# Performance work log

Measured on AMD Instinct MI355X. Metric: run time of the kernel, lower is better.

Reference implementation:

```python
import jax, jax.numpy as jnp
import numpy as np

D_IN = 512
HLS = [1024, 1024, 512]
N_Q = 4096
N_K = 16384
N_CLASSES = 100
BN_EPS = 1e-5


def _bn(x, gamma, beta):
    # BatchNorm1d in training mode: per-batch mean/biased-var normalization
    m = jnp.mean(x, axis=0)
    v = jnp.var(x, axis=0)
    return gamma * (x - m) * jax.lax.rsqrt(v + BN_EPS) + beta


def _neg_cdist(a, b):
    # -||a_i - b_j||_2 via expanded form (GEMM-dominated)
    a2 = jnp.sum(a * a, axis=1, keepdims=True)          # [N,1]
    b2 = jnp.sum(b * b, axis=1, keepdims=True).T        # [1,M]
    d2 = a2 + b2 - 2.0 * (a @ b.T)                      # [N,M]
    return -jnp.sqrt(jnp.maximum(d2, 0.0))


def setup_inputs() -> dict:
    key = jax.random.key(0)
    ks = jax.random.split(key, 32)
    inp = {
        "x": jax.random.normal(ks[0], (N_Q, D_IN), jnp.float32),
        "x_n": jax.random.normal(ks[1], (N_K, D_IN), jnp.float32),
        "y_n": jax.random.randint(ks[2], (N_K,), 0, N_CLASSES, jnp.int32),
        "in_gamma": jnp.ones((D_IN,), jnp.float32),
        "in_beta": jnp.zeros((D_IN,), jnp.float32),
    }
    dims = [D_IN] + HLS
    ki = 3
    for i in range(len(HLS)):
        fan_in = dims[i]
        bound = 1.0 / np.sqrt(fan_in)
        inp[f"W{i}"] = jax.random.uniform(ks[ki], (dims[i + 1], dims[i]), jnp.float32, -bound, bound); ki += 1
        inp[f"b{i}"] = jax.random.uniform(ks[ki], (dims[i + 1],), jnp.float32, -bound, bound); ki += 1
        inp[f"g{i}"] = jnp.ones((dims[i + 1],), jnp.float32)
        inp[f"bt{i}"] = jnp.zeros((dims[i + 1],), jnp.float32)
    return inp


def reference(x, x_n, y_n, in_gamma, in_beta,
              W0, b0, g0, bt0, W1, b1, g1, bt1, W2, b2, g2, bt2):
    x = _bn(x, in_gamma, in_beta)
    x_n = _bn(x_n, in_gamma, in_beta)
    layers = [(W0, b0, g0, bt0), (W1, b1, g1, bt1), (W2, b2, g2, bt2)]
    for W, b, g, bt in layers:
        x = _bn(jnp.tanh(x @ W.T + b), g, bt)
        x_n = _bn(jnp.tanh(x_n @ W.T + b), g, bt)
    sim = _neg_cdist(x, x_n)                       # [N_Q, N_K]
    scores = jax.nn.softmax(sim, axis=1)
    y_ohe = jax.nn.one_hot(y_n, N_CLASSES, dtype=x.dtype)  # [N_K, C]
    return jnp.clip(scores @ y_ohe, 0.0, 1.0)
```

## Files before the change

kernel.cpp:

```cpp
#include <hip/hip_runtime.h>
#include <math.h>

#define NQ 4096
#define NK 16384
#define NROWS 20480
#define NCLS 100
#define PCLS 112
#define DCH 16

typedef __attribute__((ext_vector_type(8))) short bf16x8;
typedef __attribute__((ext_vector_type(4))) float f32x4;

__device__ inline unsigned short f2bf(float f) {
  unsigned u = __float_as_uint(f);
  u += 0x7fff + ((u >> 16) & 1);
  return (unsigned short)(u >> 16);
}
__device__ inline void upk(unsigned u, float& a, float& b) {
  a = __uint_as_float(u << 16);
  b = __uint_as_float(u & 0xffff0000u);
}
__device__ inline float fast_tanh(float x) {
  float e = __expf(2.f * x);
  return 1.f - 2.f / (e + 1.f);
}
__device__ inline void gload_lds16(const unsigned short* g, unsigned short* l) {
  __builtin_amdgcn_global_load_lds(
      (const __attribute__((address_space(1))) unsigned int*)g,
      (__attribute__((address_space(3))) unsigned int*)l, 16, 0, 0);
}

__global__ __launch_bounds__(256) void conv_bf16(
    const float* __restrict__ in, unsigned short* __restrict__ outp, size_t n4) {
  size_t i = (size_t)blockIdx.x * 256 + threadIdx.x;
  size_t stride = (size_t)gridDim.x * 256;
  for (; i < n4; i += stride) {
    float4 v = ((const float4*)in)[i];
    unsigned lo = (unsigned)f2bf(v.x) | ((unsigned)f2bf(v.y) << 16);
    unsigned hi = (unsigned)f2bf(v.z) | ((unsigned)f2bf(v.w) << 16);
    ((uint2*)outp)[i] = make_uint2(lo, hi);
  }
}

__global__ __launch_bounds__(256) void colstats_part_f(
    const float* __restrict__ A, int D, int rpc, float* __restrict__ part) {
  int j = blockIdx.x * 256 + threadIdx.x;
  int c = blockIdx.y;
  const float* p = A + (size_t)c * rpc * D + j;
  float s = 0.f, s2 = 0.f;
#pragma unroll 4
  for (int r = 0; r < rpc; ++r) {
    float v = p[(size_t)r * D];
    s += v; s2 += v * v;
  }
  part[(size_t)c * 2 * D + j] = s;
  part[(size_t)c * 2 * D + D + j] = s2;
}

__global__ __launch_bounds__(256) void finish_ab(
    const float* __restrict__ part, int D, float invN,
    const float* __restrict__ g, const float* __restrict__ bt,
    float* __restrict__ ab) {
  int j = blockIdx.x * 256 + threadIdx.x;
  if (j >= D) return;
  float s = 0.f, s2 = 0.f;
  for (int c = 0; c < 64; ++c) {
    s += part[(size_t)c * 2 * D + j];
    s2 += part[(size_t)c * 2 * D + D + j];
  }
  float m = s * invN;
  float v = fmaxf(s2 * invN - m * m, 0.f);
  float a = g[j] * rsqrtf(v + 1e-5f);
  ab[2 * j] = a;
  ab[2 * j + 1] = bt[j] - a * m;
}

__global__ __launch_bounds__(256) void ab_from_stats(
    const float* __restrict__ st, const float* __restrict__ g,
    const float* __restrict__ bt, float invN, float* __restrict__ ab, int M) {
  int j = blockIdx.x * 256 + threadIdx.x;
  if (j >= M) return;
  float s = st[2 * j], s2 = st[2 * j + 1];
  float m = s * invN;
  float v = fmaxf(s2 * invN - m * m, 0.f);
  float a = g[j] * rsqrtf(v + 1e-5f);
  ab[2 * j] = a;
  ab[2 * j + 1] = bt[j] - a * m;
}

__global__ __launch_bounds__(256) void fold_w(
    const float* __restrict__ W, const float* __restrict__ b,
    const float* __restrict__ ab, int K,
    unsigned short* __restrict__ Wo, float* __restrict__ bo) {
  int j = blockIdx.x;
  int t = threadIdx.x;
  const float* Wr = W + (size_t)j * K;
  unsigned short* Wor = Wo + (size_t)j * K;
  float s = 0.f;
  for (int k = t; k < K; k += 256) {
    float w = Wr[k];
    Wor[k] = f2bf(ab[2 * k] * w);
    s += ab[2 * k + 1] * w;
  }
  __shared__ float red[4];
#pragma unroll
  for (int off = 32; off; off >>= 1) s += __shfl_down(s, off, 64);
  if ((t & 63) == 0) red[t >> 6] = s;
  __syncthreads();
  if (t == 0) bo[j] = b[j] + red[0] + red[1] + red[2] + red[3];
}

__global__ __launch_bounds__(256) void gemm_v6(
    const unsigned short* __restrict__ A, const unsigned short* __restrict__ W,
    const float* __restrict__ bias, unsigned short* __restrict__ C,
    float* __restrict__ st, int M, int K) {
  __shared__ unsigned short As[4][128 * 32];
  __shared__ unsigned short Ws[4][128 * 32];
  int tid = threadIdx.x;
  int l = tid & 63, w = tid >> 6;
  int rowBase = blockIdx.y * 128, colBase = blockIdx.x * 128;
  int rowOff = (w >> 1) * 64, colOff = (w & 1) * 64;
  int fr = l & 15, fc = l >> 4;

  const unsigned short* Ag[2];
  const unsigned short* Wg[2];
  int slot[2];
#pragma unroll
  for (int j = 0; j < 2; ++j) {
    int i = tid + j * 256;
    int r = i >> 2, c = (i & 3) ^ (r & 3);
    slot[j] = i * 8;
    Ag[j] = A + (size_t)(rowBase + r) * K + c * 8;
    Wg[j] = W + (size_t)(colBase + r) * K + c * 8;
  }
  auto stage = [&](int s, int bb) {
    int ko = s * 32;
#pragma unroll
    for (int j = 0; j < 2; ++j) {
      gload_lds16(Ag[j] + ko, &As[bb][0] + slot[j]);
      gload_lds16(Wg[j] + ko, &Ws[bb][0] + slot[j]);
    }
  };

  f32x4 acc[4][4];
#pragma unroll
  for (int m = 0; m < 4; ++m)
#pragma unroll
    for (int n = 0; n < 4; ++n) acc[m][n] = (f32x4){0.f, 0.f, 0.f, 0.f};

  int NS = K >> 5;
  stage(0, 0);
  stage(1, 1);
  stage(2, 2);
  for (int s = 0; s < NS; ++s) {
    if (s + 2 < NS) {
      asm volatile("s_waitcnt vmcnt(8)" ::: "memory");
    } else if (s + 1 < NS) {
      asm volatile("s_waitcnt vmcnt(4)" ::: "memory");
    } else {
      asm volatile("s_waitcnt vmcnt(0)" ::: "memory");
    }
    __builtin_amdgcn_s_barrier();
    __builtin_amdgcn_sched_barrier(0);
    int b = s & 3;
    bf16x8 av[4], bv[4];
#pragma unroll
    for (int m = 0; m < 4; ++m) {
      int row = rowOff + m * 16 + fr;
      int p = fc ^ (row & 3);
      av[m] = *(const bf16x8*)((const char*)&As[b][0] + row * 64 + p * 16);
    }
#pragma unroll
    for (int n = 0; n < 4; ++n) {
      int row = colOff + n * 16 + fr;
      int p = fc ^ (row & 3);
      bv[n] = *(const bf16x8*)((const char*)&Ws[b][0] + row * 64 + p * 16);
    }
    if (s + 3 < NS) stage(s + 3, (s + 3) & 3);
#pragma unroll
    for (int m = 0; m < 4; ++m)
#pragma unroll
      for (int n = 0; n < 4; ++n)
        acc[m][n] = __builtin_amdgcn_mfma_f32_16x16x32_bf16(av[m], bv[n], acc[m][n], 0, 0, 0);
  }

  float ts1[4] = {0.f, 0.f, 0.f, 0.f};
  float ts2[4] = {0.f, 0.f, 0.f, 0.f};
#pragma unroll
  for (int m = 0; m < 4; ++m) {
#pragma unroll
    for (int r = 0; r < 4; ++r) {
      size_t row = rowBase + rowOff + m * 16 + fc * 4 + r;
      unsigned short* Crow = C + row * M;
#pragma unroll
      for (int n = 0; n < 4; ++n) {
        int col = colBase + colOff + n * 16 + fr;
        float val = fast_tanh(acc[m][n][r] + bias[col]);
        Crow[col] = f2bf(val);
        ts1[n] += val;
        ts2[n] += val * val;
      }
    }
  }
#pragma unroll
  for (int n = 0; n < 4; ++n) {
    float s1 = ts1[n], s2 = ts2[n];
    s1 += __shfl_xor(s1, 16, 64); s1 += __shfl_xor(s1, 32, 64);
    s2 += __shfl_xor(s2, 16, 64); s2 += __shfl_xor(s2, 32, 64);
    if (fc == 0) {
      int col = colBase + colOff + n * 16 + fr;
      atomicAdd(&st[2 * col], s1);
      atomicAdd(&st[2 * col + 1], s2);
    }
  }
}

__global__ __launch_bounds__(256) void bn_final(
    unsigned short* __restrict__ F, const float* __restrict__ ab,
    float* __restrict__ norms) {
  int w = threadIdx.x >> 6, l = threadIdx.x & 63;
  int row = blockIdx.x * 4 + w;
  unsigned short* p = F + (size_t)row * 512 + l * 8;
  uint4 v = *(const uint4*)p;
  int j0 = l * 8;
  float f[8];
  upk(v.x, f[0], f[1]); upk(v.y, f[2], f[3]);
  upk(v.z, f[4], f[5]); upk(v.w, f[6], f[7]);
  float s = 0.f;
  unsigned pk[4];
#pragma unroll
  for (int e = 0; e < 8; e += 2) {
    float a0 = ab[2 * (j0 + e)] * f[e] + ab[2 * (j0 + e) + 1];
    float a1 = ab[2 * (j0 + e + 1)] * f[e + 1] + ab[2 * (j0 + e + 1) + 1];
    s += a0 * a0 + a1 * a1;
    pk[e >> 1] = (unsigned)f2bf(a0) | ((unsigned)f2bf(a1) << 16);
  }
  *(uint4*)p = make_uint4(pk[0], pk[1], pk[2], pk[3]);
#pragma unroll
  for (int off = 32; off; off >>= 1) s += __shfl_down(s, off, 64);
  if (l == 0) norms[row] = s;
}

__global__ __launch_bounds__(256) void scatter_ohe(
    const int* __restrict__ yn, unsigned short* __restrict__ oheT) {
  int k = blockIdx.x * 256 + threadIdx.x;
  if (k < NK) oheT[(size_t)yn[k] * NK + k] = 0x3F80;
}

__global__ __launch_bounds__(512, 2) void dist_v5(
    const unsigned short* __restrict__ F,
    const float* __restrict__ norms,
    const unsigned short* __restrict__ oheT,
    float* __restrict__ part) {
  __shared__ unsigned short kbuf[3][128 * 64];
  __shared__ unsigned short Qs[8 * 64 * 64];
  __shared__ unsigned short Ps[64][136];
  __shared__ float k2s[1024];
  int tid = threadIdx.x;
  int l = tid & 63, w = tid >> 6;
  int qBase = blockIdx.x * 64;
  int kBase0 = blockIdx.y * 1024;
  int mg = w & 1, ng = w >> 1;
  int qtw = w & 3, cth = w >> 2;
  int fr = l & 15, fc = l >> 4;

  for (int i = tid; i < 1024; i += 512) k2s[i] = norms[NQ + kBase0 + i];
  float q2r0 = norms[qBase + mg * 32 + fr];
  float q2r1 = norms[qBase + mg * 32 + 16 + fr];
  __builtin_amdgcn_sched_barrier(0);

#pragma unroll
  for (int j = 0; j < 8; ++j) {
    int i = tid + j * 512;
    int ss = i >> 9;
    int row = (i >> 3) & 63;
    int c = (i & 7) ^ (row & 7);
    gload_lds16(F + (size_t)(qBase + row) * 512 + ss * 64 + c * 8, Qs + i * 8);
  }

  int i0 = tid, i1 = tid + 512;
  int r0 = i0 >> 3, c0 = (i0 & 7) ^ (r0 & 7);
  int r1 = i1 >> 3, c1 = (i1 & 7) ^ (r1 & 7);
  auto stage = [&](int slice, int bb) {
    int kRow = kBase0 + (slice >> 3) * 128;
    int ko = (slice & 7) * 64;
    gload_lds16(F + (size_t)(NQ + kRow + r0) * 512 + ko + c0 * 8,
                &kbuf[bb][0] + i0 * 8);
    gload_lds16(F + (size_t)(NQ + kRow + r1) * 512 + ko + c1 * 8,
                &kbuf[bb][0] + i1 * 8);
  };

  f32x4 accC[4];
#pragma unroll
  for (int c = 0; c < 4; ++c) accC[c] = (f32x4){0.f, 0.f, 0.f, 0.f};

  stage(0, 0);
  stage(1, 1);
  asm volatile("s_waitcnt lgkmcnt(0)" ::: "memory");

  for (int kt = 0; kt < 8; ++kt) {
    f32x4 acc[2][2];
#pragma unroll
    for (int t2 = 0; t2 < 2; ++t2)
#pragma unroll
      for (int qt = 0; qt < 2; ++qt) acc[t2][qt] = (f32x4){0.f, 0.f, 0.f, 0.f};
    bf16x8 ob[4][4];
#pragma unroll
    for (int kc = 0; kc < 4; ++kc)
#pragma unroll
      for (int c = 0; c < 4; ++c) ob[kc][c] = (bf16x8){0, 0, 0, 0, 0, 0, 0, 0};
#pragma unroll
    for (int s = 0; s < 8; ++s) {
      int slice = kt * 8 + s;
      if (slice == 63) {
        asm volatile("s_waitcnt vmcnt(0)" ::: "memory");
      } else if (s == 1 || s == 2) {
        asm volatile("s_waitcnt vmcnt(18)" ::: "memory");
      } else {
        asm volatile("s_waitcnt vmcnt(2)" ::: "memory");
      }
      __builtin_amdgcn_s_barrier();
      __builtin_amdgcn_sched_barrier(0);
      int b = slice % 3;
      bf16x8 kv[2][2];
#pragma unroll
      for (int kc = 0; kc < 2; ++kc)
#pragma unroll
        for (int t2 = 0; t2 < 2; ++t2) {
          int row = ng * 32 + t2 * 16 + fr;
          int sl = (kc * 4 + fc) ^ (row & 7);
          kv[kc][t2] = *(const bf16x8*)((const char*)&kbuf[b][0] + row * 128 + sl * 16);
        }
      bf16x8 avx[2][2];
#pragma unroll
      for (int kc = 0; kc < 2; ++kc)
#pragma unroll
        for (int qt = 0; qt < 2; ++qt) {
          int row = mg * 32 + qt * 16 + fr;
          int sl = (kc * 4 + fc) ^ (fr & 7);
          avx[kc][qt] = *(const bf16x8*)((const char*)Qs + s * 8192 + row * 128 + sl * 16);
        }
      if (slice + 2 < 64) stage(slice + 2, (slice + 2) % 3);
      if (s == 0) {
        __builtin_amdgcn_sched_barrier(0);
#pragma unroll
        for (int kc = 0; kc < 4; ++kc)
#pragma unroll
          for (int c = 0; c < 4; ++c) {
            int ctg = cth * 4 + c;
            if (ctg < 7)
              ob[kc][c] = *(const bf16x8*)(
                  oheT + (size_t)(ctg * 16 + fr) * NK + kBase0 + kt * 128 + kc * 32 + fc * 8);
          }
        __builtin_amdgcn_sched_barrier(0);
      }
#pragma unroll
      for (int kc = 0; kc < 2; ++kc)
#pragma unroll
        for (int t2 = 0; t2 < 2; ++t2)
#pragma unroll
          for (int qt = 0; qt < 2; ++qt)
            acc[t2][qt] = __builtin_amdgcn_mfma_f32_16x16x32_bf16(
                kv[kc][t2], avx[kc][qt], acc[t2][qt], 0, 0, 0);
    }
#pragma unroll
    for (int t2 = 0; t2 < 2; ++t2) {
      float k2v[4];
#pragma unroll
      for (int r = 0; r < 4; ++r)
        k2v[r] = k2s[kt * 128 + ng * 32 + t2 * 16 + fc * 4 + r];
#pragma unroll
      for (int qt = 0; qt < 2; ++qt) {
        int q = mg * 32 + qt * 16 + fr;
        float q2 = qt ? q2r1 : q2r0;
        float pv[4];
#pragma unroll
        for (int r = 0; r < 4; ++r) {
          float d2 = q2 + k2v[r] - 2.f * acc[t2][qt][r];
          pv[r] = __expf(-sqrtf(fmaxf(d2, 0.f)));
        }
        unsigned lo = (unsigned)f2bf(pv[0]) | ((unsigned)f2bf(pv[1]) << 16);
        unsigned hi = (unsigned)f2bf(pv[2]) | ((unsigned)f2bf(pv[3]) << 16);
        *(uint2*)(&Ps[q][ng * 32 + t2 * 16 + fc * 4]) = make_uint2(lo, hi);
      }
    }
    asm volatile("s_waitcnt lgkmcnt(0)" ::: "memory");
    __builtin_amdgcn_s_barrier();
    __builtin_amdgcn_sched_barrier(0);
#pragma unroll
    for (int kc = 0; kc < 4; ++kc) {
      bf16x8 pa = *(const bf16x8*)(&Ps[qtw * 16 + fr][kc * 32 + fc * 8]);
#pragma unroll
      for (int c = 0; c < 4; ++c) {
        int ctg = cth * 4 + c;
        if (ctg < 7)
          accC[c] = __builtin_amdgcn_mfma_f32_16x16x32_bf16(pa, ob[kc][c], accC[c], 0, 0, 0);
      }
    }
  }
#pragma unroll
  for (int c = 0; c < 4; ++c) {
    int ctg = cth * 4 + c;
    if (ctg < 7) {
#pragma unroll
      for (int r = 0; r < 4; ++r) {
        int q = qBase + qtw * 16 + fc * 4 + r;
        part[((size_t)q * DCH + blockIdx.y) * PCLS + ctg * 16 + fr] = accC[c][r];
      }
    }
  }
}

__global__ __launch_bounds__(128) void combine_out(
    const float* __restrict__ part, float* __restrict__ outp) {
  int q = blockIdx.x;
  int t = threadIdx.x;
  float num = 0.f;
  if (t < NCLS) {
#pragma unroll
    for (int ch = 0; ch < DCH; ++ch)
      num += part[((size_t)q * DCH + ch) * PCLS + t];
  }
  __shared__ float sn[128];
  sn[t] = (t < NCLS) ? num : 0.f;
  __syncthreads();
#pragma unroll
  for (int off = 64; off; off >>= 1) {
    if (t < off) sn[t] += sn[t + off];
    __syncthreads();
  }
  float L = sn[0];
  if (t < NCLS) outp[(size_t)q * NCLS + t] = fminf(fmaxf(num / L, 0.f), 1.f);
}

extern "C" void kernel_launch(void* const* d_in, const int* in_sizes, int n_in,
                              void* d_out, int out_size, void* d_ws, size_t ws_size,
                              hipStream_t stream) {
  (void)in_sizes; (void)n_in; (void)out_size; (void)ws_size;
  const float* x   = (const float*)d_in[0];
  const float* xn  = (const float*)d_in[1];
  const int*   yn  = (const int*)d_in[2];
  const float* ing = (const float*)d_in[3];
  const float* inb = (const float*)d_in[4];
  const float* Wl[3]  = {(const float*)d_in[5], (const float*)d_in[9],  (const float*)d_in[13]};
  const float* bl[3]  = {(const float*)d_in[6], (const float*)d_in[10], (const float*)d_in[14]};
  const float* gl[3]  = {(const float*)d_in[7], (const float*)d_in[11], (const float*)d_in[15]};
  const float* btl[3] = {(const float*)d_in[8], (const float*)d_in[12], (const float*)d_in[16]};
  float* outp = (float*)d_out;

  unsigned short* featA = (unsigned short*)d_ws;
  unsigned short* featB = featA + (size_t)NROWS * 1024;
  unsigned short* wq  = featB + (size_t)NROWS * 1024;
  unsigned short* wk  = wq + (size_t)1024 * 1024;
  unsigned short* ohe = wk + (size_t)1024 * 1024;
  float* spart = (float*)(ohe + (size_t)PCLS * NK);
  float* abq   = spart + 64 * 2 * 512;
  float* abk   = abq + 2048;
  float* statq = abk + 2048;
  float* statk = statq + 2048;
  float* bpq   = statk + 2048;
  float* bpk   = bpq + 1024;
  float* norms = bpk + 1024;
  float* part  = norms + NROWS;

  colstats_part_f<<<dim3(2, 64), 256, 0, stream>>>(x, 512, NQ / 64, spart);
  finish_ab<<<2, 256, 0, stream>>>(spart, 512, 1.0f / NQ, ing, inb, abq);
  colstats_part_f<<<dim3(2, 64), 256, 0, stream>>>(xn, 512, NK / 64, spart);
  finish_ab<<<2, 256, 0, stream>>>(spart, 512, 1.0f / NK, ing, inb, abk);

  conv_bf16<<<1024, 256, 0, stream>>>(x, featA, (size_t)NQ * 512 / 4);
  conv_bf16<<<2048, 256, 0, stream>>>(xn, featA + (size_t)NQ * 512, (size_t)NK * 512 / 4);

  hipMemsetAsync(ohe, 0, (size_t)PCLS * NK * sizeof(unsigned short), stream);
  scatter_ohe<<<NK / 256, 256, 0, stream>>>(yn, ohe);

  int dims[4] = {512, 1024, 1024, 512};
  unsigned short *src = featA, *dst = featB;
  for (int lyr = 0; lyr < 3; ++lyr) {
    int K = dims[lyr], M = dims[lyr + 1];
    fold_w<<<M, 256, 0, stream>>>(Wl[lyr], bl[lyr], abq, K, wq, bpq);
    fold_w<<<M, 256, 0, stream>>>(Wl[lyr], bl[lyr], abk, K, wk, bpk);
    hipMemsetAsync(statq, 0, (size_t)M * 2 * sizeof(float), stream);
    hipMemsetAsync(statk, 0, (size_t)M * 2 * sizeof(float), stream);
    gemm_v6<<<dim3(M / 128, NQ / 128), 256, 0, stream>>>(src, wq, bpq, dst, statq, M, K);
    gemm_v6<<<dim3(M / 128, NK / 128), 256, 0, stream>>>(
        src + (size_t)NQ * K, wk, bpk, dst + (size_t)NQ * M, statk, M, K);
    ab_from_stats<<<M / 256, 256, 0, stream>>>(statq, gl[lyr], btl[lyr], 1.0f / NQ, abq, M);
    ab_from_stats<<<M / 256, 256, 0, stream>>>(statk, gl[lyr], btl[lyr], 1.0f / NK, abk, M);
    unsigned short* t = src; src = dst; dst = t;
  }
  bn_final<<<NQ / 4, 256, 0, stream>>>(src, abq, norms);
  bn_final<<<NK / 4, 256, 0, stream>>>(src + (size_t)NQ * 512, abk, norms + NQ);

  dist_v5<<<dim3(NQ / 64, DCH), 512, 0, stream>>>(src, norms, ohe, part);
  combine_out<<<NQ, 128, 0, stream>>>(part, outp);
}
```

Baseline: 566.2 us.

## Restructure GEMM and distance main loops to process two K-slices per barrier

Both the MLP GEMM and the distance kernel now wait for all outstanding loads and synchronise once per pair of K-slices instead of once per slice. Each pair issues the next two slice prefetches right after the barrier, then runs a larger MFMA burst under raised wave priority (s_setprio). The distance kernel grows its K buffer from three to four stages and replaces the predicated one-hot loads with clamped unconditional loads. The GEMM also gains a launch bound of two blocks per SM. The aim is fewer barriers and longer uninterrupted MFMA runs, at the cost of a shallower effective prefetch lead (vmcnt(0) every pair), more registers and more LDS.

```diff
diff --git a/kernel.cpp b/kernel.cpp
--- a/kernel.cpp
+++ b/kernel.cpp
@@ -110,7 +110,7 @@
   if (t == 0) bo[j] = b[j] + red[0] + red[1] + red[2] + red[3];
 }
 
-__global__ __launch_bounds__(256) void gemm_v6(
+__global__ __launch_bounds__(256, 2) void gemm_v6(
     const unsigned short* __restrict__ A, const unsigned short* __restrict__ W,
     const float* __restrict__ bias, unsigned short* __restrict__ C,
     float* __restrict__ st, int M, int K) {
@@ -148,40 +148,45 @@
 #pragma unroll
     for (int n = 0; n < 4; ++n) acc[m][n] = (f32x4){0.f, 0.f, 0.f, 0.f};
 
-  int NS = K >> 5;
+  int NP = K >> 6;
   stage(0, 0);
   stage(1, 1);
-  stage(2, 2);
-  for (int s = 0; s < NS; ++s) {
-    if (s + 2 < NS) {
-      asm volatile("s_waitcnt vmcnt(8)" ::: "memory");
-    } else if (s + 1 < NS) {
-      asm volatile("s_waitcnt vmcnt(4)" ::: "memory");
-    } else {
-      asm volatile("s_waitcnt vmcnt(0)" ::: "memory");
-    }
+  for (int P = 0; P < NP; ++P) {
+    asm volatile("s_waitcnt vmcnt(0)" ::: "memory");
     __builtin_amdgcn_s_barrier();
     __builtin_amdgcn_sched_barrier(0);
-    int b = s & 3;
-    bf16x8 av[4], bv[4];
-#pragma unroll
-    for (int m = 0; m < 4; ++m) {
-      int row = rowOff + m * 16 + fr;
-      int p = fc ^ (row & 3);
-      av[m] = *(const bf16x8*)((const char*)&As[b][0] + row * 64 + p * 16);
-    }
-#pragma unroll
-    for (int n = 0; n < 4; ++n) {
-      int row = colOff + n * 16 + fr;
-      int p = fc ^ (row & 3);
-      bv[n] = *(const bf16x8*)((const char*)&Ws[b][0] + row * 64 + p * 16);
-    }
-    if (s + 3 < NS) stage(s + 3, (s + 3) & 3);
-#pragma unroll
-    for (int m = 0; m < 4; ++m)
-#pragma unroll
-      for (int n = 0; n < 4; ++n)
-        acc[m][n] = __builtin_amdgcn_mfma_f32_16x16x32_bf16(av[m], bv[n], acc[m][n], 0, 0, 0);
+    if (P + 1 < NP) {
+      stage(2 * P + 2, (2 * P + 2) & 3);
+      stage(2 * P + 3, (2 * P + 3) & 3);
+    }
+    __builtin_amdgcn_sched_barrier(0);
+    bf16x8 av[2][4], bv[2][4];
+#pragma unroll
+    for (int sl2 = 0; sl2 < 2; ++sl2) {
+      int b = (2 * P + sl2) & 3;
+#pragma unroll
+      for (int m = 0; m < 4; ++m) {
+        int row = rowOff + m * 16 + fr;
+        int p = fc ^ (row & 3);
+        av[sl2][m] = *(const bf16x8*)((const char*)&As[b][0] + row * 64 + p * 16);
+      }
+#pragma unroll
+      for (int n = 0; n < 4; ++n) {
+        int row = colOff + n * 16 + fr;
+        int p = fc ^ (row & 3);
+        bv[sl2][n] = *(const bf16x8*)((const char*)&Ws[b][0] + row * 64 + p * 16);
+      }
+    }
+    __builtin_amdgcn_s_setprio(1);
+#pragma unroll
+    for (int sl2 = 0; sl2 < 2; ++sl2)
+#pragma unroll
+      for (int m = 0; m < 4; ++m)
+#pragma unroll
+        for (int n = 0; n < 4; ++n)
+          acc[m][n] = __builtin_amdgcn_mfma_f32_16x16x32_bf16(
+              av[sl2][m], bv[sl2][n], acc[m][n], 0, 0, 0);
+    __builtin_amdgcn_s_setprio(0);
   }
 
   float ts1[4] = {0.f, 0.f, 0.f, 0.f};
@@ -252,7 +257,7 @@
     const float* __restrict__ norms,
     const unsigned short* __restrict__ oheT,
     float* __restrict__ part) {
-  __shared__ unsigned short kbuf[3][128 * 64];
+  __shared__ unsigned short kbuf[4][128 * 64];
   __shared__ unsigned short Qs[8 * 64 * 64];
   __shared__ unsigned short Ps[64][136];
   __shared__ float k2s[1024];
@@ -306,62 +311,60 @@
       for (int qt = 0; qt < 2; ++qt) acc[t2][qt] = (f32x4){0.f, 0.f, 0.f, 0.f};
     bf16x8 ob[4][4];
 #pragma unroll
-    for (int kc = 0; kc < 4; ++kc)
-#pragma unroll
-      for (int c = 0; c < 4; ++c) ob[kc][c] = (bf16x8){0, 0, 0, 0, 0, 0, 0, 0};
-#pragma unroll
-    for (int s = 0; s < 8; ++s) {
-      int slice = kt * 8 + s;
-      if (slice == 63) {
-        asm volatile("s_waitcnt vmcnt(0)" ::: "memory");
-      } else if (s == 1 || s == 2) {
-        asm volatile("s_waitcnt vmcnt(18)" ::: "memory");
-      } else {
-        asm volatile("s_waitcnt vmcnt(2)" ::: "memory");
-      }
+    for (int P = 0; P < 4; ++P) {
+      int gp = kt * 4 + P;
+      asm volatile("s_waitcnt vmcnt(0)" ::: "memory");
       __builtin_amdgcn_s_barrier();
       __builtin_amdgcn_sched_barrier(0);
-      int b = slice % 3;
-      bf16x8 kv[2][2];
-#pragma unroll
-      for (int kc = 0; kc < 2; ++kc)
-#pragma unroll
-        for (int t2 = 0; t2 < 2; ++t2) {
-          int row = ng * 32 + t2 * 16 + fr;
-          int sl = (kc * 4 + fc) ^ (row & 7);
-          kv[kc][t2] = *(const bf16x8*)((const char*)&kbuf[b][0] + row * 128 + sl * 16);
-        }
-      bf16x8 avx[2][2];
-#pragma unroll
-      for (int kc = 0; kc < 2; ++kc)
-#pragma unroll
-        for (int qt = 0; qt < 2; ++qt) {
-          int row = mg * 32 + qt * 16 + fr;
-          int sl = (kc * 4 + fc) ^ (fr & 7);
-          avx[kc][qt] = *(const bf16x8*)((const char*)Qs + s * 8192 + row * 128 + sl * 16);
-        }
-      if (slice + 2 < 64) stage(slice + 2, (slice + 2) % 3);
-      if (s == 0) {
-        __builtin_amdgcn_sched_barrier(0);
+      if (gp + 1 < 32) {
+        stage(2 * gp + 2, (2 * gp + 2) & 3);
+        stage(2 * gp + 3, (2 * gp + 3) & 3);
+      }
+      if (P == 0) {
 #pragma unroll
         for (int kc = 0; kc < 4; ++kc)
 #pragma unroll
           for (int c = 0; c < 4; ++c) {
             int ctg = cth * 4 + c;
-            if (ctg < 7)
-              ob[kc][c] = *(const bf16x8*)(
-                  oheT + (size_t)(ctg * 16 + fr) * NK + kBase0 + kt * 128 + kc * 32 + fc * 8);
+            int ctgl = ctg < 7 ? ctg : 6;
+            ob[kc][c] = *(const bf16x8*)(
+                oheT + (size_t)(ctgl * 16 + fr) * NK + kBase0 + kt * 128 + kc * 32 + fc * 8);
           }
-        __builtin_amdgcn_sched_barrier(0);
-      }
-#pragma unroll
-      for (int kc = 0; kc < 2; ++kc)
-#pragma unroll
-        for (int t2 = 0; t2 < 2; ++t2)
-#pragma unroll
-          for (int qt = 0; qt < 2; ++qt)
-            acc[t2][qt] = __builtin_amdgcn_mfma_f32_16x16x32_bf16(
-                kv[kc][t2], avx[kc][qt], acc[t2][qt], 0, 0, 0);
+      }
+      __builtin_amdgcn_sched_barrier(0);
+      bf16x8 kv[2][2][2], avx[2][2][2];
+#pragma unroll
+      for (int sl2 = 0; sl2 < 2; ++sl2) {
+        int sIn = P * 2 + sl2;
+        int b = (2 * gp + sl2) & 3;
+#pragma unroll
+        for (int kc = 0; kc < 2; ++kc) {
+#pragma unroll
+          for (int t2 = 0; t2 < 2; ++t2) {
+            int row = ng * 32 + t2 * 16 + fr;
+            int sl = (kc * 4 + fc) ^ (row & 7);
+            kv[sl2][kc][t2] = *(const bf16x8*)((const char*)&kbuf[b][0] + row * 128 + sl * 16);
+          }
+#pragma unroll
+          for (int qt = 0; qt < 2; ++qt) {
+            int row = mg * 32 + qt * 16 + fr;
+            int sl = (kc * 4 + fc) ^ (fr & 7);
+            avx[sl2][kc][qt] = *(const bf16x8*)((const char*)Qs + sIn * 8192 + row * 128 + sl * 16);
+          }
+        }
+      }
+      __builtin_amdgcn_s_setprio(1);
+#pragma unroll
+      for (int sl2 = 0; sl2 < 2; ++sl2)
+#pragma unroll
+        for (int kc = 0; kc < 2; ++kc)
+#pragma unroll
+          for (int t2 = 0; t2 < 2; ++t2)
+#pragma unroll
+            for (int qt = 0; qt < 2; ++qt)
+              acc[t2][qt] = __builtin_amdgcn_mfma_f32_16x16x32_bf16(
+                  kv[sl2][kc][t2], avx[sl2][kc][qt], acc[t2][qt], 0, 0, 0);
+      __builtin_amdgcn_s_setprio(0);
     }
 #pragma unroll
     for (int t2 = 0; t2 < 2; ++t2) {
```

New measurement: 619.5 us. 1.09x slower.

## Shrink distance tile to 32 queries, hold query fragments in registers

Applied to the files above, without the earlier changes.

The fused distance/softmax/class-sum kernel now processes 32 query rows per block instead of 64. Each wave keeps its whole query row fragment (16 bf16x8 vectors) in registers rather than staging it through a 64KB LDS buffer. Launch bounds are raised to 4 blocks per CU, the one-hot loads move after the distance MFMAs, and the K-slice prefetch for the next tile is issued after the class accumulation. This frees LDS and aims for higher occupancy, but every key tile is now loaded by twice as many blocks, doubling key traffic, and register pressure rises.

```diff
diff --git a/kernel.cpp b/kernel.cpp
--- a/kernel.cpp
+++ b/kernel.cpp
@@ -247,36 +247,32 @@
   if (k < NK) oheT[(size_t)yn[k] * NK + k] = 0x3F80;
 }
 
-__global__ __launch_bounds__(512, 2) void dist_v5(
+__global__ __launch_bounds__(512, 4) void dist_v7(
     const unsigned short* __restrict__ F,
     const float* __restrict__ norms,
     const unsigned short* __restrict__ oheT,
     float* __restrict__ part) {
   __shared__ unsigned short kbuf[3][128 * 64];
-  __shared__ unsigned short Qs[8 * 64 * 64];
-  __shared__ unsigned short Ps[64][136];
+  __shared__ unsigned short Ps[32][136];
   __shared__ float k2s[1024];
   int tid = threadIdx.x;
   int l = tid & 63, w = tid >> 6;
-  int qBase = blockIdx.x * 64;
+  int qBase = blockIdx.x * 32;
   int kBase0 = blockIdx.y * 1024;
-  int mg = w & 1, ng = w >> 1;
-  int qtw = w & 3, cth = w >> 2;
+  int qt = w & 1, ng = w >> 1;
+  int cth = w >> 1;
   int fr = l & 15, fc = l >> 4;
 
   for (int i = tid; i < 1024; i += 512) k2s[i] = norms[NQ + kBase0 + i];
-  float q2r0 = norms[qBase + mg * 32 + fr];
-  float q2r1 = norms[qBase + mg * 32 + 16 + fr];
+  float q2r = norms[qBase + qt * 16 + fr];
+
+  bf16x8 av[16];
+  {
+    const unsigned short* rowp = F + (size_t)(qBase + qt * 16 + fr) * 512 + fc * 8;
+#pragma unroll
+    for (int g = 0; g < 16; ++g) av[g] = *(const bf16x8*)(rowp + g * 32);
+  }
   __builtin_amdgcn_sched_barrier(0);
-
-#pragma unroll
-  for (int j = 0; j < 8; ++j) {
-    int i = tid + j * 512;
-    int ss = i >> 9;
-    int row = (i >> 3) & 63;
-    int c = (i & 7) ^ (row & 7);
-    gload_lds16(F + (size_t)(qBase + row) * 512 + ss * 64 + c * 8, Qs + i * 8);
-  }
 
   int i0 = tid, i1 = tid + 512;
   int r0 = i0 >> 3, c0 = (i0 & 7) ^ (r0 & 7);
@@ -290,32 +286,23 @@
                 &kbuf[bb][0] + i1 * 8);
   };
 
-  f32x4 accC[4];
-#pragma unroll
-  for (int c = 0; c < 4; ++c) accC[c] = (f32x4){0.f, 0.f, 0.f, 0.f};
+  f32x4 accC[2];
+#pragma unroll
+  for (int c = 0; c < 2; ++c) accC[c] = (f32x4){0.f, 0.f, 0.f, 0.f};
 
   stage(0, 0);
   stage(1, 1);
   asm volatile("s_waitcnt lgkmcnt(0)" ::: "memory");
 
   for (int kt = 0; kt < 8; ++kt) {
-    f32x4 acc[2][2];
-#pragma unroll
-    for (int t2 = 0; t2 < 2; ++t2)
-#pragma unroll
-      for (int qt = 0; qt < 2; ++qt) acc[t2][qt] = (f32x4){0.f, 0.f, 0.f, 0.f};
-    bf16x8 ob[4][4];
-#pragma unroll
-    for (int kc = 0; kc < 4; ++kc)
-#pragma unroll
-      for (int c = 0; c < 4; ++c) ob[kc][c] = (bf16x8){0, 0, 0, 0, 0, 0, 0, 0};
+    f32x4 acc[2];
+#pragma unroll
+    for (int t2 = 0; t2 < 2; ++t2) acc[t2] = (f32x4){0.f, 0.f, 0.f, 0.f};
 #pragma unroll
     for (int s = 0; s < 8; ++s) {
       int slice = kt * 8 + s;
-      if (slice == 63) {
+      if (s == 7) {
         asm volatile("s_waitcnt vmcnt(0)" ::: "memory");
-      } else if (s == 1 || s == 2) {
-        asm volatile("s_waitcnt vmcnt(18)" ::: "memory");
       } else {
         asm volatile("s_waitcnt vmcnt(2)" ::: "memory");
       }
@@ -331,80 +318,65 @@
           int sl = (kc * 4 + fc) ^ (row & 7);
           kv[kc][t2] = *(const bf16x8*)((const char*)&kbuf[b][0] + row * 128 + sl * 16);
         }
-      bf16x8 avx[2][2];
+      if (s < 6) stage(slice + 2, (slice + 2) % 3);
 #pragma unroll
       for (int kc = 0; kc < 2; ++kc)
 #pragma unroll
-        for (int qt = 0; qt < 2; ++qt) {
-          int row = mg * 32 + qt * 16 + fr;
-          int sl = (kc * 4 + fc) ^ (fr & 7);
-          avx[kc][qt] = *(const bf16x8*)((const char*)Qs + s * 8192 + row * 128 + sl * 16);
-        }
-      if (slice + 2 < 64) stage(slice + 2, (slice + 2) % 3);
-      if (s == 0) {
-        __builtin_amdgcn_sched_barrier(0);
-#pragma unroll
-        for (int kc = 0; kc < 4; ++kc)
-#pragma unroll
-          for (int c = 0; c < 4; ++c) {
-            int ctg = cth * 4 + c;
-            if (ctg < 7)
-              ob[kc][c] = *(const bf16x8*)(
-                  oheT + (size_t)(ctg * 16 + fr) * NK + kBase0 + kt * 128 + kc * 32 + fc * 8);
-          }
-        __builtin_amdgcn_sched_barrier(0);
-      }
-#pragma unroll
-      for (int kc = 0; kc < 2; ++kc)
-#pragma unroll
         for (int t2 = 0; t2 < 2; ++t2)
-#pragma unroll
-          for (int qt = 0; qt < 2; ++qt)
-            acc[t2][qt] = __builtin_amdgcn_mfma_f32_16x16x32_bf16(
-                kv[kc][t2], avx[kc][qt], acc[t2][qt], 0, 0, 0);
-    }
+          acc[t2] = __builtin_amdgcn_mfma_f32_16x16x32_bf16(
+              kv[kc][t2], av[s * 2 + kc], acc[t2], 0, 0, 0);
+    }
+    bf16x8 ob[4][2];
+#pragma unroll
+    for (int kc = 0; kc < 4; ++kc)
+#pragma unroll
+      for (int c = 0; c < 2; ++c) {
+        int ctg = cth * 2 + c;
+        int ctgl = ctg < 7 ? ctg : 6;
+        ob[kc][c] = *(const bf16x8*)(
+            oheT + (size_t)(ctgl * 16 + fr) * NK + kBase0 + kt * 128 + kc * 32 + fc * 8);
+      }
 #pragma unroll
     for (int t2 = 0; t2 < 2; ++t2) {
       float k2v[4];
 #pragma unroll
       for (int r = 0; r < 4; ++r)
         k2v[r] = k2s[kt * 128 + ng * 32 + t2 * 16 + fc * 4 + r];
-#pragma unroll
-      for (int qt = 0; qt < 2; ++qt) {
-        int q = mg * 32 + qt * 16 + fr;
-        float q2 = qt ? q2r1 : q2r0;
-        float pv[4];
-#pragma unroll
-        for (int r = 0; r < 4; ++r) {
-          float d2 = q2 + k2v[r] - 2.f * acc[t2][qt][r];
-          pv[r] = __expf(-sqrtf(fmaxf(d2, 0.f)));
-        }
-        unsigned lo = (unsigned)f2bf(pv[0]) | ((unsigned)f2bf(pv[1]) << 16);
-        unsigned hi = (unsigned)f2bf(pv[2]) | ((unsigned)f2bf(pv[3]) << 16);
-        *(uint2*)(&Ps[q][ng * 32 + t2 * 16 + fc * 4]) = make_uint2(lo, hi);
-      }
+      float pv[4];
+#pragma unroll
+      for (int r = 0; r < 4; ++r) {
+        float d2 = q2r + k2v[r] - 2.f * acc[t2][r];
+        pv[r] = __expf(-sqrtf(fmaxf(d2, 0.f)));
+      }
+      unsigned lo = (unsigned)f2bf(pv[0]) | ((unsigned)f2bf(pv[1]) << 16);
+      unsigned hi = (unsigned)f2bf(pv[2]) | ((unsigned)f2bf(pv[3]) << 16);
+      *(uint2*)(&Ps[qt * 16 + fr][ng * 32 + t2 * 16 + fc * 4]) = make_uint2(lo, hi);
     }
     asm volatile("s_waitcnt lgkmcnt(0)" ::: "memory");
     __builtin_amdgcn_s_barrier();
     __builtin_amdgcn_sched_barrier(0);
 #pragma unroll
     for (int kc = 0; kc < 4; ++kc) {
-      bf16x8 pa = *(const bf16x8*)(&Ps[qtw * 16 + fr][kc * 32 + fc * 8]);
-#pragma unroll
-      for (int c = 0; c < 4; ++c) {
-        int ctg = cth * 4 + c;
+      bf16x8 pa = *(const bf16x8*)(&Ps[qt * 16 + fr][kc * 32 + fc * 8]);
+#pragma unroll
+      for (int c = 0; c < 2; ++c) {
+        int ctg = cth * 2 + c;
         if (ctg < 7)
           accC[c] = __builtin_amdgcn_mfma_f32_16x16x32_bf16(pa, ob[kc][c], accC[c], 0, 0, 0);
       }
     }
-  }
-#pragma unroll
-  for (int c = 0; c < 4; ++c) {
-    int ctg = cth * 4 + c;
+    if (kt < 7) {
+      stage(kt * 8 + 8, (kt * 8 + 8) % 3);
+      stage(kt * 8 + 9, (kt * 8 + 9) % 3);
+    }
+  }
+#pragma unroll
+  for (int c = 0; c < 2; ++c) {
+    int ctg = cth * 2 + c;
     if (ctg < 7) {
 #pragma unroll
       for (int r = 0; r < 4; ++r) {
-        int q = qBase + qtw * 16 + fc * 4 + r;
+        int q = qBase + qt * 16 + fc * 4 + r;
         part[((size_t)q * DCH + blockIdx.y) * PCLS + ctg * 16 + fr] = accC[c][r];
       }
     }
@@ -492,6 +464,6 @@
   bn_final<<<NQ / 4, 256, 0, stream>>>(src, abq, norms);
   bn_final<<<NK / 4, 256, 0, stream>>>(src + (size_t)NQ * 512, abk, norms + NQ);
 
-  dist_v5<<<dim3(NQ / 64, DCH), 512, 0, stream>>>(src, norms, ohe, part);
+  dist_v7<<<dim3(NQ / 32, DCH), 512, 0, stream>>>(src, norms, ohe, part);
   combine_out<<<NQ, 128, 0, stream>>>(part, outp);
 }
```

Result: slower. 678.2 us (+19.8%).
